# Kernel tuning notes

Hardware: AMD Instinct MI355X
Metric: run time of the kernel (lower is better)

## Reference

```python
import jax, jax.numpy as jnp
import numpy as np

MARGIN = 0.2


def _pairwise_distances(emb):
    # Euclidean distances with torch-style zero-masked sqrt (non-squared path).
    dot = jnp.matmul(emb, emb.T)                      # [N, N]
    sq = jnp.diagonal(dot)                            # [N]
    d2 = sq[None, :] - 2.0 * dot + sq[:, None]
    d2 = jnp.maximum(d2, 0.0)
    zero_mask = (d2 == 0.0).astype(d2.dtype)
    return (1.0 - zero_mask) * jnp.sqrt(d2 + zero_mask * 1e-16)


def setup_inputs() -> dict:
    key = jax.random.key(0)
    k1, k2 = jax.random.split(key)
    N, D, C = 512, 512, 64
    labels = jax.random.randint(k1, (N,), 0, C, dtype=jnp.int64 if jax.config.jax_enable_x64 else jnp.int32)
    embeddings = jax.random.normal(k2, (N, D), dtype=jnp.float32)
    return {"labels": labels, "embeddings": embeddings}


def reference(labels, embeddings):
    # Semi-hard... actually Difficulty.Easy path of TripletLoss.forward
    N = embeddings.shape[0]
    pdist = _pairwise_distances(embeddings)                      # [N, N]
    adjacency_not = labels[None, :] != labels[:, None]           # [N, N] bool

    pdist_tile = jnp.tile(pdist, (N, 1))                         # [N*N, N]
    mask = jnp.tile(adjacency_not, (N, 1))                       # [N*N, N]
    # Easy difficulty: negatives strictly farther than the anchor-positive dist
    mask = mask & (pdist_tile > pdist.T.reshape(-1, 1))

    maskf = mask.astype(pdist.dtype)
    mask_final = (jnp.sum(maskf, axis=1, keepdims=True) > 0.0).reshape(N, N).T  # [N, N] bool

    # masked minimum over tiled rows
    axis_max = jnp.max(pdist_tile, axis=1, keepdims=True)
    neg_outside = (jnp.min((pdist_tile - axis_max) * maskf, axis=1, keepdims=True)
                   + axis_max).reshape(N, N).T                   # [N, N]

    # masked maximum over negatives per anchor
    adjf = adjacency_not.astype(pdist.dtype)
    axis_min = jnp.min(pdist, axis=1, keepdims=True)
    neg_inside = jnp.max((pdist - axis_min) * adjf, axis=1, keepdims=True) + axis_min  # [N, 1]
    neg_inside = jnp.broadcast_to(neg_inside, (N, N))

    semi_hard_negatives = jnp.where(mask_final, neg_outside, neg_inside)
    loss_mat = MARGIN + pdist - semi_hard_negatives

    eye = jnp.eye(N, dtype=bool)
    mask_positives = (labels[None, :] == labels[:, None]) & ~eye
    num_positives = jnp.sum(mask_positives).astype(loss_mat.dtype)
    loss = jnp.sum(jnp.maximum(loss_mat * mask_positives.astype(loss_mat.dtype), 0.0))
    return loss / (num_positives + 1e-8)
```

## Files before the change

### kernel.cpp

```cpp
#include <hip/hip_runtime.h>
#include <math.h>


#define NN 512
#define DD 512
#define MARGIN_F 0.2f

typedef __attribute__((ext_vector_type(8))) short bf16x8;
typedef __attribute__((ext_vector_type(4))) float f32x4;

__device__ __forceinline__ unsigned short f2bf(float x){
    unsigned u = __float_as_uint(x);
    return (unsigned short)((u + 0x7FFFu + ((u >> 16) & 1u)) >> 16);
}
__device__ __forceinline__ float bf2f(unsigned short h){
    return __uint_as_float(((unsigned)h) << 16);
}

__global__ __launch_bounds__(256) void k_prep(
    const float* __restrict__ emb,
    unsigned short* __restrict__ ehi,
    unsigned short* __restrict__ elo,
    float* __restrict__ norms,
    unsigned int* __restrict__ accums)
{
    const int tid = threadIdx.x, wave = tid >> 6, lane = tid & 63;
    const int j = blockIdx.x * 4 + wave;
    const float4* row = (const float4*)(emb + (size_t)j * DD);
    float acc = 0.f;
    #pragma unroll
    for (int i = 0; i < 2; ++i){
        const int f4i = lane + (i << 6);
        float4 v = row[f4i];
        acc = fmaf(v.x,v.x,acc); acc = fmaf(v.y,v.y,acc);
        acc = fmaf(v.z,v.z,acc); acc = fmaf(v.w,v.w,acc);
        ushort4 h, l;
        h.x = f2bf(v.x); l.x = f2bf(v.x - bf2f(h.x));
        h.y = f2bf(v.y); l.y = f2bf(v.y - bf2f(h.y));
        h.z = f2bf(v.z); l.z = f2bf(v.z - bf2f(h.z));
        h.w = f2bf(v.w); l.w = f2bf(v.w - bf2f(h.w));
        ((ushort4*)ehi)[(size_t)j * 128 + f4i] = h;
        ((ushort4*)elo)[(size_t)j * 128 + f4i] = l;
    }
    #pragma unroll
    for (int o = 32; o > 0; o >>= 1) acc += __shfl_xor(acc, o, 64);
    if (lane == 0) norms[j] = acc;
    if (blockIdx.x == 0 && tid < 3) accums[tid] = 0u;
}

__global__ __launch_bounds__(256) void k_dist(
    const unsigned short* __restrict__ ehi,
    const unsigned short* __restrict__ elo,
    const float* __restrict__ norms,
    float* __restrict__ Dm)
{
    __shared__ short sh[4][32][136];
    const int tid = threadIdx.x;
    const int bi = blockIdx.y, bj = blockIdx.x;
    const int wave = tid >> 6, lane = tid & 63;
    const int rowb = (wave >> 1) * 16, colb = (wave & 1) * 16;
    const int fr = lane & 15;
    const int koff0 = (lane >> 4) * 8;

    f32x4 acc = {0.f, 0.f, 0.f, 0.f};

    for (int c = 0; c < 4; ++c){
        if (c) __syncthreads();
        #pragma unroll
        for (int u = 0; u < 8; ++u){
            const int idx = tid + (u << 8);
            const int buf = idx >> 9;
            const int w = idx & 511;
            const int r = w >> 4, c8 = w & 15;
            const unsigned short* src = (buf & 1) ? elo : ehi;
            const int rowg = ((buf >> 1) ? bj : bi) * 32 + r;
            float4 v = ((const float4*)src)[(size_t)rowg * 64 + c * 16 + c8];
            *(float4*)(&sh[buf][r][c8 << 3]) = v;
        }
        __syncthreads();
        #pragma unroll
        for (int s = 0; s < 4; ++s){
            const int k = koff0 + (s << 5);
            bf16x8 ahi = *(const bf16x8*)(&sh[0][rowb + fr][k]);
            bf16x8 alo = *(const bf16x8*)(&sh[1][rowb + fr][k]);
            bf16x8 bhi = *(const bf16x8*)(&sh[2][colb + fr][k]);
            bf16x8 blo = *(const bf16x8*)(&sh[3][colb + fr][k]);
            acc = __builtin_amdgcn_mfma_f32_16x16x32_bf16(ahi, bhi, acc, 0, 0, 0);
            acc = __builtin_amdgcn_mfma_f32_16x16x32_bf16(ahi, blo, acc, 0, 0, 0);
            acc = __builtin_amdgcn_mfma_f32_16x16x32_bf16(alo, bhi, acc, 0, 0, 0);
        }
    }
    const int colg = bj * 32 + colb + fr;
    const int rowg0 = bi * 32 + rowb + (lane >> 4) * 4;
    const float sc = norms[colg];
    #pragma unroll
    for (int reg = 0; reg < 4; ++reg){
        const int rowg = rowg0 + reg;
        const float d2 = norms[rowg] + sc - 2.f * acc[reg];
        Dm[(size_t)rowg * NN + colg] = sqrtf(fmaxf(d2, 0.f));
    }
}

__global__ __launch_bounds__(256) void k_mine(
    const int* __restrict__ labels,
    const float* __restrict__ Dm,
    float* __restrict__ accums,
    float* __restrict__ out,
    int nblocks)
{
    __shared__ int slbl[NN];
    __shared__ float drow[4][NN];
    __shared__ unsigned short plist[4][128];
    __shared__ int pcnt[4];

    const int tid = threadIdx.x, wave = tid >> 6, lane = tid & 63;
    const int j = blockIdx.x * 4 + wave;

    slbl[tid] = labels[tid];
    slbl[tid + 256] = labels[tid + 256];
    if (tid < 4) pcnt[tid] = 0;
    __syncthreads();

    const float4* rp = (const float4*)(Dm + (size_t)j * NN);
    const float4 va = rp[lane * 2], vb = rp[lane * 2 + 1];
    *(float4*)(&drow[wave][lane * 8]) = va;
    *(float4*)(&drow[wave][lane * 8 + 4]) = vb;
    float d[8] = {va.x, va.y, va.z, va.w, vb.x, vb.y, vb.z, vb.w};
    const int lj = slbl[j];
    int lb[8];
    #pragma unroll
    for (int m = 0; m < 8; ++m) lb[m] = slbl[lane * 8 + m];

    #pragma unroll
    for (int m = 0; m < 8; ++m){
        const int k = lane * 8 + m;
        if (k != j && lb[m] == lj){
            const int ix = atomicAdd(&pcnt[wave], 1);
            plist[wave][ix] = (unsigned short)k;
        }
    }
    float vmaxl = 0.f;
    #pragma unroll
    for (int m = 0; m < 8; ++m) if (lb[m] != lj) vmaxl = fmaxf(vmaxl, d[m]);
    #pragma unroll
    for (int o = 32; o > 0; o >>= 1) vmaxl = fmaxf(vmaxl, __shfl_xor(vmaxl, o, 64));

    const int np = pcnt[wave];
    float wloss = 0.f;
    for (int p = 0; p < np; ++p){
        const int a = plist[wave][p];
        const float dpa = drow[wave][a];
        float vm = 1e30f;
        #pragma unroll
        for (int m = 0; m < 8; ++m){
            const bool cnd = (lb[m] != lj) && (d[m] > dpa);
            vm = cnd ? fminf(vm, d[m]) : vm;
        }
        #pragma unroll
        for (int o = 32; o > 0; o >>= 1) vm = fminf(vm, __shfl_xor(vm, o, 64));
        const float neg = (vm < 1e29f) ? vm : vmaxl;
        const float term = MARGIN_F + dpa - neg;
        if (lane == 0 && term > 0.f) wloss += term;
    }
    if (lane == 0){
        if (wloss != 0.f) atomicAdd(&accums[0], wloss);
        if (np) atomicAdd((unsigned int*)&accums[1], (unsigned int)np);
    }
    __syncthreads();
    if (tid == 0){
        __threadfence();
        const unsigned old = atomicAdd((unsigned int*)&accums[2], 1u);
        if (old == (unsigned)(nblocks - 1)){
            const float L = atomicAdd(&accums[0], 0.f);
            const unsigned C = atomicAdd((unsigned int*)&accums[1], 0u);
            out[0] = L / ((float)C + 1e-8f);
        }
    }
}

extern "C" void kernel_launch(void* const* d_in, const int* in_sizes, int n_in,
                              void* d_out, int out_size, void* d_ws, size_t ws_size,
                              hipStream_t stream) {
    (void)in_sizes; (void)n_in; (void)out_size; (void)ws_size;
    const int* labels = (const int*)d_in[0];
    const float* emb  = (const float*)d_in[1];
    char* ws = (char*)d_ws;
    float*          Dm     = (float*)ws;
    unsigned short* ehi    = (unsigned short*)(ws + (1u << 20));
    unsigned short* elo    = (unsigned short*)(ws + (1u << 20) + (1u << 19));
    float*          norms  = (float*)(ws + (1u << 21));
    unsigned int*   accums = (unsigned int*)(ws + (1u << 21) + 4096u);

    k_prep<<<128, 256, 0, stream>>>(emb, ehi, elo, norms, accums);
    k_dist<<<dim3(16, 16), 256, 0, stream>>>(ehi, elo, norms, Dm);
    k_mine<<<128, 256, 0, stream>>>(labels, Dm, (float*)accums, (float*)d_out, 128);
}
```

Measured before the change: 80.51 us.

## Fuse prep, distance and mining kernels into one with last-block-per-row mining

```diff
diff --git a/kernel.cpp b/kernel.cpp
--- a/kernel.cpp
+++ b/kernel.cpp
@@ -3,8 +3,8 @@
 
 
 #define NN 512
-#define DD 512
 #define MARGIN_F 0.2f
+#define LK 520
 
 typedef __attribute__((ext_vector_type(8))) short bf16x8;
 typedef __attribute__((ext_vector_type(4))) float f32x4;
@@ -17,162 +17,161 @@
     return __uint_as_float(((unsigned)h) << 16);
 }
 
-__global__ __launch_bounds__(256) void k_prep(
+__global__ __launch_bounds__(256, 1) void k_fused(
+    const int* __restrict__ labels,
     const float* __restrict__ emb,
-    unsigned short* __restrict__ ehi,
-    unsigned short* __restrict__ elo,
-    float* __restrict__ norms,
-    unsigned int* __restrict__ accums)
+    float* __restrict__ Dm,
+    int* __restrict__ ctrl,
+    float* __restrict__ out)
 {
-    const int tid = threadIdx.x, wave = tid >> 6, lane = tid & 63;
-    const int j = blockIdx.x * 4 + wave;
-    const float4* row = (const float4*)(emb + (size_t)j * DD);
-    float acc = 0.f;
+    __shared__ __align__(16) char sm[133376];
+    short* sh  = (short*)sm;
+    float* snI = (float*)(sm + 133120);
+    float* snJ = snI + 32;
+    int* slbl            = (int*)sm;
+    float* drow          = (float*)(sm + 2048);
+    unsigned short* plist = (unsigned short*)(sm + 2048 + 8192);
+    int* pcnt            = (int*)(sm + 2048 + 8192 + 1024);
+    int* sflag           = pcnt + 4;
+
+    const int tid  = threadIdx.x;
+    const int wave = tid >> 6, lane = tid & 63;
+    const int bi = blockIdx.x >> 4, bj = blockIdx.x & 15;
+
+    {
+        const int row = tid >> 3;
+        const int s8  = tid & 7;
+        const float4* Ep = (const float4*)emb;
+        float ssI = 0.f, ssJ = 0.f;
+        #pragma unroll
+        for (int i = 0; i < 16; ++i) {
+            const int c4 = s8 + (i << 3);
+            const float4 vI = Ep[(size_t)(bi * 32 + row) * 128 + c4];
+            const float4 vJ = Ep[(size_t)(bj * 32 + row) * 128 + c4];
+            ssI = fmaf(vI.x, vI.x, ssI); ssI = fmaf(vI.y, vI.y, ssI);
+            ssI = fmaf(vI.z, vI.z, ssI); ssI = fmaf(vI.w, vI.w, ssI);
+            ssJ = fmaf(vJ.x, vJ.x, ssJ); ssJ = fmaf(vJ.y, vJ.y, ssJ);
+            ssJ = fmaf(vJ.z, vJ.z, ssJ); ssJ = fmaf(vJ.w, vJ.w, ssJ);
+            ushort4 h, l;
+            h.x = f2bf(vI.x); l.x = f2bf(vI.x - bf2f(h.x));
+            h.y = f2bf(vI.y); l.y = f2bf(vI.y - bf2f(h.y));
+            h.z = f2bf(vI.z); l.z = f2bf(vI.z - bf2f(h.z));
+            h.w = f2bf(vI.w); l.w = f2bf(vI.w - bf2f(h.w));
+            *(ushort4*)(&sh[(0 * 32 + row) * LK + (c4 << 2)]) = h;
+            *(ushort4*)(&sh[(1 * 32 + row) * LK + (c4 << 2)]) = l;
+            h.x = f2bf(vJ.x); l.x = f2bf(vJ.x - bf2f(h.x));
+            h.y = f2bf(vJ.y); l.y = f2bf(vJ.y - bf2f(h.y));
+            h.z = f2bf(vJ.z); l.z = f2bf(vJ.z - bf2f(h.z));
+            h.w = f2bf(vJ.w); l.w = f2bf(vJ.w - bf2f(h.w));
+            *(ushort4*)(&sh[(2 * 32 + row) * LK + (c4 << 2)]) = h;
+            *(ushort4*)(&sh[(3 * 32 + row) * LK + (c4 << 2)]) = l;
+        }
+        ssI += __shfl_xor(ssI, 1, 64); ssJ += __shfl_xor(ssJ, 1, 64);
+        ssI += __shfl_xor(ssI, 2, 64); ssJ += __shfl_xor(ssJ, 2, 64);
+        ssI += __shfl_xor(ssI, 4, 64); ssJ += __shfl_xor(ssJ, 4, 64);
+        if (s8 == 0) { snI[row] = ssI; snJ[row] = ssJ; }
+    }
+    __syncthreads();
+
+    const int rowb = (wave >> 1) << 4, colb = (wave & 1) << 4;
+    const int fr = lane & 15;
+    const int k0 = (lane >> 4) << 3;
+    f32x4 acc = {0.f, 0.f, 0.f, 0.f};
     #pragma unroll
-    for (int i = 0; i < 2; ++i){
-        const int f4i = lane + (i << 6);
-        float4 v = row[f4i];
-        acc = fmaf(v.x,v.x,acc); acc = fmaf(v.y,v.y,acc);
-        acc = fmaf(v.z,v.z,acc); acc = fmaf(v.w,v.w,acc);
-        ushort4 h, l;
-        h.x = f2bf(v.x); l.x = f2bf(v.x - bf2f(h.x));
-        h.y = f2bf(v.y); l.y = f2bf(v.y - bf2f(h.y));
-        h.z = f2bf(v.z); l.z = f2bf(v.z - bf2f(h.z));
-        h.w = f2bf(v.w); l.w = f2bf(v.w - bf2f(h.w));
-        ((ushort4*)ehi)[(size_t)j * 128 + f4i] = h;
-        ((ushort4*)elo)[(size_t)j * 128 + f4i] = l;
+    for (int t8 = 0; t8 < 16; ++t8) {
+        const int k = k0 + (t8 << 5);
+        bf16x8 ahi = *(const bf16x8*)(&sh[(0 * 32 + rowb + fr) * LK + k]);
+        bf16x8 alo = *(const bf16x8*)(&sh[(1 * 32 + rowb + fr) * LK + k]);
+        bf16x8 bhi = *(const bf16x8*)(&sh[(2 * 32 + colb + fr) * LK + k]);
+        bf16x8 blo = *(const bf16x8*)(&sh[(3 * 32 + colb + fr) * LK + k]);
+        acc = __builtin_amdgcn_mfma_f32_16x16x32_bf16(ahi, bhi, acc, 0, 0, 0);
+        acc = __builtin_amdgcn_mfma_f32_16x16x32_bf16(ahi, blo, acc, 0, 0, 0);
+        acc = __builtin_amdgcn_mfma_f32_16x16x32_bf16(alo, bhi, acc, 0, 0, 0);
     }
-    #pragma unroll
-    for (int o = 32; o > 0; o >>= 1) acc += __shfl_xor(acc, o, 64);
-    if (lane == 0) norms[j] = acc;
-    if (blockIdx.x == 0 && tid < 3) accums[tid] = 0u;
-}
-
-__global__ __launch_bounds__(256) void k_dist(
-    const unsigned short* __restrict__ ehi,
-    const unsigned short* __restrict__ elo,
-    const float* __restrict__ norms,
-    float* __restrict__ Dm)
-{
-    __shared__ short sh[4][32][136];
-    const int tid = threadIdx.x;
-    const int bi = blockIdx.y, bj = blockIdx.x;
-    const int wave = tid >> 6, lane = tid & 63;
-    const int rowb = (wave >> 1) * 16, colb = (wave & 1) * 16;
-    const int fr = lane & 15;
-    const int koff0 = (lane >> 4) * 8;
-
-    f32x4 acc = {0.f, 0.f, 0.f, 0.f};
-
-    for (int c = 0; c < 4; ++c){
-        if (c) __syncthreads();
+    {
+        const int colg = bj * 32 + colb + fr;
+        const float sc = snJ[colb + fr];
+        const int rl0 = rowb + ((lane >> 4) << 2);
         #pragma unroll
-        for (int u = 0; u < 8; ++u){
-            const int idx = tid + (u << 8);
-            const int buf = idx >> 9;
-            const int w = idx & 511;
-            const int r = w >> 4, c8 = w & 15;
-            const unsigned short* src = (buf & 1) ? elo : ehi;
-            const int rowg = ((buf >> 1) ? bj : bi) * 32 + r;
-            float4 v = ((const float4*)src)[(size_t)rowg * 64 + c * 16 + c8];
-            *(float4*)(&sh[buf][r][c8 << 3]) = v;
-        }
-        __syncthreads();
-        #pragma unroll
-        for (int s = 0; s < 4; ++s){
-            const int k = koff0 + (s << 5);
-            bf16x8 ahi = *(const bf16x8*)(&sh[0][rowb + fr][k]);
-            bf16x8 alo = *(const bf16x8*)(&sh[1][rowb + fr][k]);
-            bf16x8 bhi = *(const bf16x8*)(&sh[2][colb + fr][k]);
-            bf16x8 blo = *(const bf16x8*)(&sh[3][colb + fr][k]);
-            acc = __builtin_amdgcn_mfma_f32_16x16x32_bf16(ahi, bhi, acc, 0, 0, 0);
-            acc = __builtin_amdgcn_mfma_f32_16x16x32_bf16(ahi, blo, acc, 0, 0, 0);
-            acc = __builtin_amdgcn_mfma_f32_16x16x32_bf16(alo, bhi, acc, 0, 0, 0);
+        for (int reg = 0; reg < 4; ++reg) {
+            const int rl = rl0 + reg;
+            const float d2 = snI[rl] + sc - 2.f * acc[reg];
+            Dm[(size_t)(bi * 32 + rl) * NN + colg] = sqrtf(fmaxf(d2, 0.f));
         }
     }
-    const int colg = bj * 32 + colb + fr;
-    const int rowg0 = bi * 32 + rowb + (lane >> 4) * 4;
-    const float sc = norms[colg];
-    #pragma unroll
-    for (int reg = 0; reg < 4; ++reg){
-        const int rowg = rowg0 + reg;
-        const float d2 = norms[rowg] + sc - 2.f * acc[reg];
-        Dm[(size_t)rowg * NN + colg] = sqrtf(fmaxf(d2, 0.f));
+
+    __syncthreads();
+    if (tid == 0) {
+        __threadfence();
+        const int o = atomicAdd(&ctrl[bi], 1);
+        *sflag = (o == 15);
     }
-}
-
-__global__ __launch_bounds__(256) void k_mine(
-    const int* __restrict__ labels,
-    const float* __restrict__ Dm,
-    float* __restrict__ accums,
-    float* __restrict__ out,
-    int nblocks)
-{
-    __shared__ int slbl[NN];
-    __shared__ float drow[4][NN];
-    __shared__ unsigned short plist[4][128];
-    __shared__ int pcnt[4];
-
-    const int tid = threadIdx.x, wave = tid >> 6, lane = tid & 63;
-    const int j = blockIdx.x * 4 + wave;
+    __syncthreads();
+    if (!*sflag) return;
+    __threadfence();
 
     slbl[tid] = labels[tid];
     slbl[tid + 256] = labels[tid + 256];
-    if (tid < 4) pcnt[tid] = 0;
     __syncthreads();
 
-    const float4* rp = (const float4*)(Dm + (size_t)j * NN);
-    const float4 va = rp[lane * 2], vb = rp[lane * 2 + 1];
-    *(float4*)(&drow[wave][lane * 8]) = va;
-    *(float4*)(&drow[wave][lane * 8 + 4]) = vb;
-    float d[8] = {va.x, va.y, va.z, va.w, vb.x, vb.y, vb.z, vb.w};
-    const int lj = slbl[j];
     int lb[8];
     #pragma unroll
     for (int m = 0; m < 8; ++m) lb[m] = slbl[lane * 8 + m];
 
-    #pragma unroll
-    for (int m = 0; m < 8; ++m){
-        const int k = lane * 8 + m;
-        if (k != j && lb[m] == lj){
-            const int ix = atomicAdd(&pcnt[wave], 1);
-            plist[wave][ix] = (unsigned short)k;
+    float wloss = 0.f;
+    unsigned wcnt = 0;
+    for (int rr = 0; rr < 8; ++rr) {
+        const int j = bi * 32 + (wave << 3) + rr;
+        const float4* rp = (const float4*)(Dm + (size_t)j * NN);
+        const float4 va = rp[lane * 2], vb = rp[lane * 2 + 1];
+        *(float4*)(&drow[wave * NN + lane * 8])     = va;
+        *(float4*)(&drow[wave * NN + lane * 8 + 4]) = vb;
+        const float d[8] = {va.x, va.y, va.z, va.w, vb.x, vb.y, vb.z, vb.w};
+        const int lj = slbl[j];
+        if (lane == 0) pcnt[wave] = 0;
+        #pragma unroll
+        for (int m = 0; m < 8; ++m) {
+            const int k = lane * 8 + m;
+            if (k != j && lb[m] == lj) {
+                const int ix = atomicAdd(&pcnt[wave], 1);
+                plist[wave * 128 + ix] = (unsigned short)k;
+            }
+        }
+        float vmaxl = 0.f;
+        #pragma unroll
+        for (int m = 0; m < 8; ++m) if (lb[m] != lj) vmaxl = fmaxf(vmaxl, d[m]);
+        #pragma unroll
+        for (int o = 32; o > 0; o >>= 1) vmaxl = fmaxf(vmaxl, __shfl_xor(vmaxl, o, 64));
+        const int np = pcnt[wave];
+        wcnt += (unsigned)np;
+        for (int p = 0; p < np; ++p) {
+            const int a = plist[wave * 128 + p];
+            const float dpa = drow[wave * NN + a];
+            float vm = 1e30f;
+            #pragma unroll
+            for (int m = 0; m < 8; ++m) {
+                const bool c = (lb[m] != lj) && (d[m] > dpa);
+                vm = c ? fminf(vm, d[m]) : vm;
+            }
+            #pragma unroll
+            for (int o = 32; o > 0; o >>= 1) vm = fminf(vm, __shfl_xor(vm, o, 64));
+            const float neg = (vm < 1e29f) ? vm : vmaxl;
+            const float term = MARGIN_F + dpa - neg;
+            if (lane == 0 && term > 0.f) wloss += term;
         }
     }
-    float vmaxl = 0.f;
-    #pragma unroll
-    for (int m = 0; m < 8; ++m) if (lb[m] != lj) vmaxl = fmaxf(vmaxl, d[m]);
-    #pragma unroll
-    for (int o = 32; o > 0; o >>= 1) vmaxl = fmaxf(vmaxl, __shfl_xor(vmaxl, o, 64));
-
-    const int np = pcnt[wave];
-    float wloss = 0.f;
-    for (int p = 0; p < np; ++p){
-        const int a = plist[wave][p];
-        const float dpa = drow[wave][a];
-        float vm = 1e30f;
-        #pragma unroll
-        for (int m = 0; m < 8; ++m){
-            const bool cnd = (lb[m] != lj) && (d[m] > dpa);
-            vm = cnd ? fminf(vm, d[m]) : vm;
-        }
-        #pragma unroll
-        for (int o = 32; o > 0; o >>= 1) vm = fminf(vm, __shfl_xor(vm, o, 64));
-        const float neg = (vm < 1e29f) ? vm : vmaxl;
-        const float term = MARGIN_F + dpa - neg;
-        if (lane == 0 && term > 0.f) wloss += term;
-    }
-    if (lane == 0){
-        if (wloss != 0.f) atomicAdd(&accums[0], wloss);
-        if (np) atomicAdd((unsigned int*)&accums[1], (unsigned int)np);
+    if (lane == 0) {
+        if (wloss != 0.f) atomicAdd((float*)&ctrl[17], wloss);
+        if (wcnt) atomicAdd((unsigned int*)&ctrl[18], wcnt);
     }
     __syncthreads();
-    if (tid == 0){
+    if (tid == 0) {
         __threadfence();
-        const unsigned old = atomicAdd((unsigned int*)&accums[2], 1u);
-        if (old == (unsigned)(nblocks - 1)){
-            const float L = atomicAdd(&accums[0], 0.f);
-            const unsigned C = atomicAdd((unsigned int*)&accums[1], 0u);
+        const int o = atomicAdd(&ctrl[16], 1);
+        if (o == 15) {
+            __threadfence();
+            const float L = atomicAdd((float*)&ctrl[17], 0.f);
+            const unsigned C = atomicAdd((unsigned int*)&ctrl[18], 0u);
             out[0] = L / ((float)C + 1e-8f);
         }
     }
@@ -185,13 +184,9 @@
     const int* labels = (const int*)d_in[0];
     const float* emb  = (const float*)d_in[1];
     char* ws = (char*)d_ws;
-    float*          Dm     = (float*)ws;
-    unsigned short* ehi    = (unsigned short*)(ws + (1u << 20));
-    unsigned short* elo    = (unsigned short*)(ws + (1u << 20) + (1u << 19));
-    float*          norms  = (float*)(ws + (1u << 21));
-    unsigned int*   accums = (unsigned int*)(ws + (1u << 21) + 4096u);
+    float* Dm  = (float*)ws;
+    int*   ctrl = (int*)(ws + (1u << 20));
 
-    k_prep<<<128, 256, 0, stream>>>(emb, ehi, elo, norms, accums);
-    k_dist<<<dim3(16, 16), 256, 0, stream>>>(ehi, elo, norms, Dm);
-    k_mine<<<128, 256, 0, stream>>>(labels, Dm, (float*)accums, (float*)d_out, 128);
+    hipMemsetAsync(ctrl, 0, 128, stream);
+    k_fused<<<256, 256, 0, stream>>>(labels, emb, Dm, ctrl, (float*)d_out);
 }
```

Measured after the change: 109.9 us. +36.5%, slower.
